# Kernel optimization log

Measured on AMD Instinct MI355X. Metric: run time of the kernel, lower is better.

The kernel has to match this reference:

```python
import jax, jax.numpy as jnp
import numpy as np

FR = 44100          # frame_rate
L = 882000          # sound length (20 s @ 44.1 kHz)
T = 2048            # number of onset time steps
H_GRU = 3
H_LSTM = 10


def setup_inputs() -> dict:
    key = jax.random.key(0)
    ks = jax.random.split(key, 20)

    def unif(k, shape, fan):
        b = 1.0 / np.sqrt(fan)
        return jax.random.uniform(k, shape, jnp.float32, -b, b)

    return {
        "sound": jax.random.normal(ks[0], (1, L), jnp.float32),
        "alpha": jnp.sort(jax.random.randint(ks[1], (1, T), 0, L), axis=1),
        # GRU (input_size=FR, hidden=3): gates ordered (r, z, n). W_hh is
        # multiplied by h0=0 (seq_len==1), so only its bias b_hh matters.
        "gru_w_ih": unif(ks[2], (3 * H_GRU, FR), H_GRU),
        "gru_b_ih": unif(ks[3], (3 * H_GRU,), H_GRU),
        "gru_b_hh": unif(ks[4], (3 * H_GRU,), H_GRU),
        "conv2_w": unif(ks[5], (32, 1, 3), 1 * 3),
        "conv2_b": unif(ks[6], (32,), 1 * 3),
        "conv3_w": unif(ks[7], (16, 32, 3), 32 * 3),
        "conv3_b": unif(ks[8], (16,), 32 * 3),
        "lin_w": unif(ks[9], (10, 17), 17),
        "lin_b": unif(ks[10], (10,), 17),
        # LSTMCell gates ordered (i, f, g, o)
        "lstm_w_ih": unif(ks[11], (4 * H_LSTM, 10), H_LSTM),
        "lstm_w_hh": unif(ks[12], (4 * H_LSTM, H_LSTM), H_LSTM),
        "lstm_b_ih": unif(ks[13], (4 * H_LSTM,), H_LSTM),
        "lstm_b_hh": unif(ks[14], (4 * H_LSTM,), H_LSTM),
        "lin1_w": unif(ks[15], (32, 10), 10),
        "lin1_b": unif(ks[16], (32,), 10),
        "lin2_w": unif(ks[17], (1, 32), 32),
        "lin2_b": unif(ks[18], (1,), 32),
    }


def _conv1d(x, w, b, pad):
    # x: (N, C_in, W), w: (C_out, C_in, K)
    y = jax.lax.conv_general_dilated(
        x, w, window_strides=(1,), padding=[(pad, pad)],
        dimension_numbers=("NCH", "OIH", "NCH"))
    return y + b[None, :, None]


def reference(sound, alpha, gru_w_ih, gru_b_ih, gru_b_hh,
              conv2_w, conv2_b, conv3_w, conv3_b, lin_w, lin_b,
              lstm_w_ih, lstm_w_hh, lstm_b_ih, lstm_b_hh,
              lin1_w, lin1_b, lin2_w, lin2_b):
    fr2 = FR // 2
    padded = jnp.pad(sound[0], (fr2, fr2))                       # (L + FR,)
    # Vectorized dynamic-window gather: one (T, FR) fragment matrix.
    idx = alpha[0][:, None] + jnp.arange(FR)[None, :]            # (T, FR)
    frags = jnp.abs(padded[idx])                                 # (T, FR)

    # GRU: batch=1 -> unbatched input of seq_len=1, h0=0 => single step.
    gi = frags @ gru_w_ih.T + gru_b_ih                           # (T, 9)
    r = jax.nn.sigmoid(gi[:, 0:3] + gru_b_hh[0:3])
    z = jax.nn.sigmoid(gi[:, 3:6] + gru_b_hh[3:6])
    n = jnp.tanh(gi[:, 6:9] + r * gru_b_hh[6:9])
    h = (1.0 - z) * n                                            # (T, 3)

    x = h[:, None, :]                                            # (T, 1, 3)
    x = jax.nn.relu(_conv1d(x, conv2_w, conv2_b, pad=1))         # (T, 32, 3)
    x = _conv1d(x, conv3_w, conv3_b, pad=0)                      # (T, 16, 1)
    feat = x[:, :, 0]                                            # (T, 16)

    a = alpha[0].astype(jnp.float32)
    intervals = jnp.concatenate([a[:1], a[1:] - a[:-1]])         # (T,)
    xin = jnp.concatenate([intervals[:, None], feat], axis=1)    # (T, 17)
    xin = xin @ lin_w.T + lin_b                                  # (T, 10)

    def step(carry, xt):
        hh, cc = carry
        g = xt @ lstm_w_ih.T + lstm_b_ih + hh @ lstm_w_hh.T + lstm_b_hh
        i, f, gg, o = jnp.split(g, 4)
        cc = jax.nn.sigmoid(f) * cc + jax.nn.sigmoid(i) * jnp.tanh(gg)
        hh = jax.nn.sigmoid(o) * jnp.tanh(cc)
        return (hh, cc), None

    init = (jnp.zeros(H_LSTM, jnp.float32), jnp.zeros(H_LSTM, jnp.float32))
    (hT, _), _ = jax.lax.scan(step, init, xin)                   # hT: (10,)

    y = jax.nn.relu(hT[None, :] @ lin1_w.T + lin1_b)             # (1, 32)
    return jax.nn.sigmoid(y @ lin2_w.T + lin2_b)                 # (1, 1)
```

## Files before the change

kernel.cpp:

```cpp
#include <hip/hip_runtime.h>

#define FRLEN 44100
#define FR2 22050
#define LSND 882000
#define PADLEN (LSND + FRLEN)
#define TSTEPS 2048
#define ROWS 8
#define NJ4 (FRLEN/4)
#define LOG2E 1.4426950408889634f

__device__ __forceinline__ float sigmoidf_(float x){ return 1.0f/(1.0f + __expf(-x)); }

__global__ void k_prep(const float* __restrict__ sound, float* __restrict__ padded){
  int stride = gridDim.x*blockDim.x;
  for (int i = blockIdx.x*blockDim.x + threadIdx.x; i < PADLEN; i += stride){
    int s = i - FR2;
    padded[i] = (s >= 0 && s < LSND) ? fabsf(sound[s]) : 0.0f;
  }
}

__global__ __launch_bounds__(512, 2) void k_gi(const float* __restrict__ padded,
                     const int* __restrict__ alpha,
                     const float* __restrict__ w,
                     float* __restrict__ gi_out){
  const int tid = threadIdx.x;
  const int row0 = blockIdx.x * ROWS;
  int base[ROWS];
#pragma unroll
  for (int r = 0; r < ROWS; ++r) base[r] = alpha[row0 + r];
  float acc[ROWS][9];
#pragma unroll
  for (int r = 0; r < ROWS; ++r)
#pragma unroll
    for (int k = 0; k < 9; ++k) acc[r][k] = 0.0f;

  for (int jj = tid; jj < NJ4; jj += 512){
    const int j = jj*4;
    float4 f[ROWS];
#pragma unroll
    for (int r = 0; r < ROWS; ++r)
      f[r] = *reinterpret_cast<const float4*>(padded + base[r] + j);
#pragma unroll
    for (int k = 0; k < 9; ++k){
      const float4 wv = *reinterpret_cast<const float4*>(w + k*FRLEN + j);
#pragma unroll
      for (int r = 0; r < ROWS; ++r){
        acc[r][k] = fmaf(f[r].x, wv.x, acc[r][k]);
        acc[r][k] = fmaf(f[r].y, wv.y, acc[r][k]);
        acc[r][k] = fmaf(f[r].z, wv.z, acc[r][k]);
        acc[r][k] = fmaf(f[r].w, wv.w, acc[r][k]);
      }
    }
  }
#pragma unroll
  for (int m = 32; m >= 1; m >>= 1){
#pragma unroll
    for (int r = 0; r < ROWS; ++r)
#pragma unroll
      for (int k = 0; k < 9; ++k)
        acc[r][k] += __shfl_xor(acc[r][k], m, 64);
  }
  __shared__ float red[8][ROWS*9];
  const int wv_ = tid >> 6, ln = tid & 63;
  if (ln == 0){
#pragma unroll
    for (int r = 0; r < ROWS; ++r)
#pragma unroll
      for (int k = 0; k < 9; ++k) red[wv_][r*9+k] = acc[r][k];
  }
  __syncthreads();
  if (tid < ROWS*9){
    float s = 0.0f;
#pragma unroll
    for (int q = 0; q < 8; ++q) s += red[q][tid];
    gi_out[row0*9 + tid] = s;
  }
}

__global__ void k_epi(const float* __restrict__ gi_in, const int* __restrict__ alpha,
    const float* __restrict__ gbih, const float* __restrict__ gbhh,
    const float* __restrict__ c2w, const float* __restrict__ c2b,
    const float* __restrict__ c3w, const float* __restrict__ c3b,
    const float* __restrict__ lw, const float* __restrict__ lb,
    const float* __restrict__ wih, const float* __restrict__ bih, const float* __restrict__ bhh,
    _Float16* __restrict__ pre){
  int t = blockIdx.x*blockDim.x + threadIdx.x;
  if (t >= TSTEPS) return;
  float gi[9];
#pragma unroll
  for (int k = 0; k < 9; ++k) gi[k] = gi_in[t*9+k] + gbih[k];
  float h[3];
#pragma unroll
  for (int q = 0; q < 3; ++q){
    float rr = sigmoidf_(gi[q]   + gbhh[q]);
    float zz = sigmoidf_(gi[3+q] + gbhh[3+q]);
    float nn = tanhf(gi[6+q] + rr*gbhh[6+q]);
    h[q] = (1.0f - zz)*nn;
  }
  float feat[16];
#pragma unroll
  for (int c = 0; c < 16; ++c) feat[c] = c3b[c];
  for (int ic = 0; ic < 32; ++ic){
    float w0 = c2w[ic*3+0], w1 = c2w[ic*3+1], w2 = c2w[ic*3+2], bb = c2b[ic];
    float x0 = fmaxf(bb + h[0]*w1 + h[1]*w2, 0.0f);
    float x1 = fmaxf(bb + h[0]*w0 + h[1]*w1 + h[2]*w2, 0.0f);
    float x2_ = fmaxf(bb + h[1]*w0 + h[2]*w1, 0.0f);
#pragma unroll
    for (int c = 0; c < 16; ++c){
      const float* wp = c3w + (c*32+ic)*3;
      feat[c] += x0*wp[0] + x1*wp[1] + x2_*wp[2];
    }
  }
  float interval = (float)(t == 0 ? alpha[0] : (alpha[t] - alpha[t-1]));
  float xin[10];
#pragma unroll
  for (int k = 0; k < 10; ++k){
    float s = lb[k] + interval*lw[k*17];
#pragma unroll
    for (int j = 0; j < 16; ++j) s = fmaf(feat[j], lw[k*17+1+j], s);
    xin[k] = s;
  }
#pragma unroll
  for (int k = 0; k < 40; ++k){
    float s = bih[k] + bhh[k];
#pragma unroll
    for (int i = 0; i < 10; ++i) s = fmaf(xin[i], wih[k*10+i], s);
    const float sc = (k >= 20 && k < 30) ? (-2.0f*LOG2E) : (-LOG2E);
    pre[t*40 + k] = (_Float16)(s * sc);
  }
}

#define LSTM_STEP(PREFETCH_STMT)                                              \
  {                                                                           \
    float g = (float)q0;                                                      \
    q0 = q1; q1 = q2; q2 = q3;                                                \
    PREFETCH_STMT;                                                            \
    float ga = g, gb = 0.0f;                                                  \
    _Pragma("unroll")                                                         \
    for (int i = 0; i < 5; ++i)  ga = fmaf(hs[i], w[i], ga);                  \
    _Pragma("unroll")                                                         \
    for (int i = 5; i < 10; ++i) gb = fmaf(hs[i], w[i], gb);                  \
    g = ga + gb;                                                              \
    float act = fmaf(__builtin_amdgcn_rcpf(1.0f + __builtin_amdgcn_exp2f(g)), s2, s3); \
    float g_sw = act;                                                         \
    asm("s_nop 1\n\tv_permlane32_swap_b32 %0, %1" : "+v"(act), "+v"(g_sw));   \
    float f_sw = act;                                                         \
    asm("v_permlane16_swap_b32 %0, %1" : "+v"(act), "+v"(f_sw));              \
    float o_sw = g_sw;                                                        \
    asm("v_permlane16_swap_b32 %0, %1" : "+v"(g_sw), "+v"(o_sw));             \
    float ig = act * g_sw;            \
    c = fmaf(f_sw, c, ig);                      \
    float th = fmaf(__builtin_amdgcn_rcpf(1.0f + __builtin_amdgcn_exp2f(c)), 2.0f, -1.0f); \
    float hn = o_sw * th;                                                     \
    _Pragma("unroll")                                                         \
    for (int i = 0; i < 10; ++i)                                              \
      hs[i] = __int_as_float(__builtin_amdgcn_readlane(__float_as_int(hn), i)); \
  }

__global__ __launch_bounds__(1024, 1) void k_lstm(const _Float16* __restrict__ pre,
                       const float* __restrict__ whh,
                       const float* __restrict__ l1w, const float* __restrict__ l1b,
                       const float* __restrict__ l2w, const float* __restrict__ l2b,
                       float* __restrict__ out){
  extern __shared__ _Float16 sp[];
  {
    uint4* dst = (uint4*)sp;
    const uint4* src = (const uint4*)pre;
    for (int i = threadIdx.x; i < (TSTEPS*40*2)/16; i += 1024) dst[i] = src[i];
  }
  __syncthreads();
  if (threadIdx.x >= 64) return;

  const int lane = threadIdx.x;
  const int gate = lane >> 4;
  const int unit_raw = lane & 15;
  const int unit = unit_raw < 10 ? unit_raw : 9;
  const int L40 = gate*10 + unit;
  const bool is_g = (gate == 2);
  const float kk  = -2.0f*LOG2E;
  const float wsc = is_g ? kk : (-LOG2E);
  const float s2  = is_g ? (2.0f*kk) : 1.0f;
  const float s3  = is_g ? (-kk)     : 0.0f;
  float w[10];
#pragma unroll
  for (int i = 0; i < 10; ++i) w[i] = whh[L40*10 + i] * wsc;

  float hs[10];
#pragma unroll
  for (int i = 0; i < 10; ++i) hs[i] = 0.0f;
  float c = 0.0f;

  _Float16 q0 = sp[0*40+L40], q1 = sp[1*40+L40], q2 = sp[2*40+L40], q3 = sp[3*40+L40];
#pragma unroll 4
  for (int t = 0; t < TSTEPS-4; ++t){
    LSTM_STEP(q3 = sp[(t+4)*40 + L40]);
  }
#pragma unroll
  for (int t = TSTEPS-4; t < TSTEPS; ++t){
    LSTM_STEP(;);
  }
  float z = 0.0f;
  if (lane < 32){
    float s = l1b[lane];
#pragma unroll
    for (int i = 0; i < 10; ++i) s = fmaf(hs[i], l1w[lane*10+i], s);
    z = fmaxf(s, 0.0f) * l2w[lane];
  }
#pragma unroll
  for (int m = 32; m >= 1; m >>= 1) z += __shfl_xor(z, m, 64);
  if (lane == 0) out[0] = sigmoidf_(z + l2b[0]);
}

extern "C" void kernel_launch(void* const* d_in, const int* in_sizes, int n_in,
                              void* d_out, int out_size, void* d_ws, size_t ws_size,
                              hipStream_t stream){
  const float* sound     = (const float*)d_in[0];
  const int*   alpha     = (const int*)  d_in[1];
  const float* gru_w_ih  = (const float*)d_in[2];
  const float* gru_b_ih  = (const float*)d_in[3];
  const float* gru_b_hh  = (const float*)d_in[4];
  const float* conv2_w   = (const float*)d_in[5];
  const float* conv2_b   = (const float*)d_in[6];
  const float* conv3_w   = (const float*)d_in[7];
  const float* conv3_b   = (const float*)d_in[8];
  const float* lin_w     = (const float*)d_in[9];
  const float* lin_b     = (const float*)d_in[10];
  const float* lstm_w_ih = (const float*)d_in[11];
  const float* lstm_w_hh = (const float*)d_in[12];
  const float* lstm_b_ih = (const float*)d_in[13];
  const float* lstm_b_hh = (const float*)d_in[14];
  const float* lin1_w    = (const float*)d_in[15];
  const float* lin1_b    = (const float*)d_in[16];
  const float* lin2_w    = (const float*)d_in[17];
  const float* lin2_b    = (const float*)d_in[18];

  float* padded = (float*)d_ws;
  float* gi     = padded + PADLEN;
  _Float16* pre = (_Float16*)(gi + TSTEPS*9);

  (void)hipFuncSetAttribute((const void*)k_lstm,
        hipFuncAttributeMaxDynamicSharedMemorySize, TSTEPS*40*2);

  hipLaunchKernelGGL(k_prep, dim3(2048), dim3(256), 0, stream, sound, padded);
  hipLaunchKernelGGL(k_gi, dim3(TSTEPS/ROWS), dim3(512), 0, stream, padded, alpha, gru_w_ih, gi);
  hipLaunchKernelGGL(k_epi, dim3(TSTEPS/256), dim3(256), 0, stream,
                     gi, alpha, gru_b_ih, gru_b_hh, conv2_w, conv2_b, conv3_w, conv3_b,
                     lin_w, lin_b, lstm_w_ih, lstm_b_ih, lstm_b_hh, pre);
  hipLaunchKernelGGL(k_lstm, dim3(1), dim3(1024), TSTEPS*40*2, stream,
                     pre, lstm_w_hh, lin1_w, lin1_b, lin2_w, lin2_b, (float*)d_out);
}
```

Measured before the change: 276.6 us.

## Convert GRU input projection to fp16 dot2 and fuse epilogue into gather kernel

Sound and GRU weights are pre-converted to packed fp16 pairs, with two copies of the sound (even- and odd-offset pairing) so that any alpha start offset can be read as aligned half2 pairs. The main gather-GEMV then uses fdot2 instructions, halving memory traffic and the FMA count. The GRU/conv/linear epilogue is fused into the same kernel, which removes one launch and the gi round trip. The LSTM asm has its s_nop padding tweaked. Using fp16 for the 44100-long dot products loses precision, and the per-row uint loads are scalar rather than vectorised.

```diff
diff --git a/kernel.cpp b/kernel.cpp
--- a/kernel.cpp
+++ b/kernel.cpp
@@ -6,127 +6,167 @@
 #define PADLEN (LSND + FRLEN)
 #define TSTEPS 2048
 #define ROWS 8
-#define NJ4 (FRLEN/4)
 #define LOG2E 1.4426950408889634f
 
+#define KPAD 44104
+#define WPROW (KPAD/2)
+#define NJP (WPROW/4)
+#define PAIRS 463056
+
+typedef _Float16 half2_ __attribute__((ext_vector_type(2)));
+
 __device__ __forceinline__ float sigmoidf_(float x){ return 1.0f/(1.0f + __expf(-x)); }
 
-__global__ void k_prep(const float* __restrict__ sound, float* __restrict__ padded){
-  int stride = gridDim.x*blockDim.x;
-  for (int i = blockIdx.x*blockDim.x + threadIdx.x; i < PADLEN; i += stride){
-    int s = i - FR2;
-    padded[i] = (s >= 0 && s < LSND) ? fabsf(sound[s]) : 0.0f;
-  }
-}
-
-__global__ __launch_bounds__(512, 2) void k_gi(const float* __restrict__ padded,
-                     const int* __restrict__ alpha,
-                     const float* __restrict__ w,
-                     float* __restrict__ gi_out){
-  const int tid = threadIdx.x;
-  const int row0 = blockIdx.x * ROWS;
-  int base[ROWS];
-#pragma unroll
-  for (int r = 0; r < ROWS; ++r) base[r] = alpha[row0 + r];
-  float acc[ROWS][9];
-#pragma unroll
-  for (int r = 0; r < ROWS; ++r)
-#pragma unroll
-    for (int k = 0; k < 9; ++k) acc[r][k] = 0.0f;
-
-  for (int jj = tid; jj < NJ4; jj += 512){
-    const int j = jj*4;
-    float4 f[ROWS];
-#pragma unroll
-    for (int r = 0; r < ROWS; ++r)
-      f[r] = *reinterpret_cast<const float4*>(padded + base[r] + j);
-#pragma unroll
-    for (int k = 0; k < 9; ++k){
-      const float4 wv = *reinterpret_cast<const float4*>(w + k*FRLEN + j);
-#pragma unroll
-      for (int r = 0; r < ROWS; ++r){
-        acc[r][k] = fmaf(f[r].x, wv.x, acc[r][k]);
-        acc[r][k] = fmaf(f[r].y, wv.y, acc[r][k]);
-        acc[r][k] = fmaf(f[r].z, wv.z, acc[r][k]);
-        acc[r][k] = fmaf(f[r].w, wv.w, acc[r][k]);
-      }
-    }
-  }
-#pragma unroll
-  for (int m = 32; m >= 1; m >>= 1){
-#pragma unroll
-    for (int r = 0; r < ROWS; ++r)
-#pragma unroll
-      for (int k = 0; k < 9; ++k)
-        acc[r][k] += __shfl_xor(acc[r][k], m, 64);
-  }
-  __shared__ float red[8][ROWS*9];
-  const int wv_ = tid >> 6, ln = tid & 63;
-  if (ln == 0){
-#pragma unroll
-    for (int r = 0; r < ROWS; ++r)
-#pragma unroll
-      for (int k = 0; k < 9; ++k) red[wv_][r*9+k] = acc[r][k];
-  }
-  __syncthreads();
-  if (tid < ROWS*9){
-    float s = 0.0f;
-#pragma unroll
-    for (int q = 0; q < 8; ++q) s += red[q][tid];
-    gi_out[row0*9 + tid] = s;
-  }
-}
-
-__global__ void k_epi(const float* __restrict__ gi_in, const int* __restrict__ alpha,
+__device__ __forceinline__ float dot2_(uint a, uint b, float c){
+#if __has_builtin(__builtin_amdgcn_fdot2)
+  return __builtin_amdgcn_fdot2(*(half2_*)&a, *(half2_*)&b, c, false);
+#else
+  half2_ ha = *(half2_*)&a, hb = *(half2_*)&b;
+  c = fmaf((float)ha.x, (float)hb.x, c);
+  return fmaf((float)ha.y, (float)hb.y, c);
+#endif
+}
+
+__global__ void k_prep16(const float* __restrict__ sound, const float* __restrict__ w,
+                         uint* __restrict__ pA, uint* __restrict__ pB,
+                         uint* __restrict__ wp){
+  const int stride = gridDim.x*blockDim.x;
+  for (int i = blockIdx.x*blockDim.x + threadIdx.x; i < PAIRS + 9*WPROW; i += stride){
+    if (i < PAIRS){
+      int e0 = 2*i - FR2;
+      float v0 = (e0 >= 0     && e0 < LSND)     ? fabsf(sound[e0])   : 0.0f;
+      float v1 = (e0+1 >= 0   && e0+1 < LSND)   ? fabsf(sound[e0+1]) : 0.0f;
+      float v2 = (e0+2 >= 0   && e0+2 < LSND)   ? fabsf(sound[e0+2]) : 0.0f;
+      half2_ a = { (_Float16)v0, (_Float16)v1 };
+      half2_ b = { (_Float16)v1, (_Float16)v2 };
+      pA[i] = *(uint*)&a;
+      pB[i] = *(uint*)&b;
+    } else {
+      int p = i - PAIRS;
+      int k = p / WPROW, pr = p % WPROW;
+      int j = 2*pr;
+      float v0 = (j   < FRLEN) ? w[k*FRLEN + j]   : 0.0f;
+      float v1 = (j+1 < FRLEN) ? w[k*FRLEN + j+1] : 0.0f;
+      half2_ a = { (_Float16)v0, (_Float16)v1 };
+      wp[i - PAIRS] = *(uint*)&a;
+    }
+  }
+}
+
+__global__ __launch_bounds__(512, 2) void k_front(const uint* __restrict__ pA,
+    const uint* __restrict__ pB, const uint* __restrict__ wp,
+    const int* __restrict__ alpha,
     const float* __restrict__ gbih, const float* __restrict__ gbhh,
     const float* __restrict__ c2w, const float* __restrict__ c2b,
     const float* __restrict__ c3w, const float* __restrict__ c3b,
     const float* __restrict__ lw, const float* __restrict__ lb,
     const float* __restrict__ wih, const float* __restrict__ bih, const float* __restrict__ bhh,
     _Float16* __restrict__ pre){
-  int t = blockIdx.x*blockDim.x + threadIdx.x;
-  if (t >= TSTEPS) return;
-  float gi[9];
-#pragma unroll
-  for (int k = 0; k < 9; ++k) gi[k] = gi_in[t*9+k] + gbih[k];
-  float h[3];
-#pragma unroll
-  for (int q = 0; q < 3; ++q){
-    float rr = sigmoidf_(gi[q]   + gbhh[q]);
-    float zz = sigmoidf_(gi[3+q] + gbhh[3+q]);
-    float nn = tanhf(gi[6+q] + rr*gbhh[6+q]);
-    h[q] = (1.0f - zz)*nn;
-  }
-  float feat[16];
-#pragma unroll
-  for (int c = 0; c < 16; ++c) feat[c] = c3b[c];
-  for (int ic = 0; ic < 32; ++ic){
-    float w0 = c2w[ic*3+0], w1 = c2w[ic*3+1], w2 = c2w[ic*3+2], bb = c2b[ic];
-    float x0 = fmaxf(bb + h[0]*w1 + h[1]*w2, 0.0f);
-    float x1 = fmaxf(bb + h[0]*w0 + h[1]*w1 + h[2]*w2, 0.0f);
-    float x2_ = fmaxf(bb + h[1]*w0 + h[2]*w1, 0.0f);
-#pragma unroll
-    for (int c = 0; c < 16; ++c){
-      const float* wp = c3w + (c*32+ic)*3;
-      feat[c] += x0*wp[0] + x1*wp[1] + x2_*wp[2];
-    }
-  }
-  float interval = (float)(t == 0 ? alpha[0] : (alpha[t] - alpha[t-1]));
-  float xin[10];
-#pragma unroll
-  for (int k = 0; k < 10; ++k){
-    float s = lb[k] + interval*lw[k*17];
-#pragma unroll
-    for (int j = 0; j < 16; ++j) s = fmaf(feat[j], lw[k*17+1+j], s);
-    xin[k] = s;
-  }
-#pragma unroll
-  for (int k = 0; k < 40; ++k){
-    float s = bih[k] + bhh[k];
-#pragma unroll
-    for (int i = 0; i < 10; ++i) s = fmaf(xin[i], wih[k*10+i], s);
-    const float sc = (k >= 20 && k < 30) ? (-2.0f*LOG2E) : (-LOG2E);
-    pre[t*40 + k] = (_Float16)(s * sc);
+  const int tid = threadIdx.x;
+  const int row0 = blockIdx.x * ROWS;
+  const uint* hp[ROWS];
+  int idx0[ROWS];
+#pragma unroll
+  for (int r = 0; r < ROWS; ++r){
+    int b = alpha[row0 + r];
+    hp[r] = (b & 1) ? pB : pA;
+    idx0[r] = b >> 1;
+  }
+  float acc[ROWS][9];
+#pragma unroll
+  for (int r = 0; r < ROWS; ++r)
+#pragma unroll
+    for (int k = 0; k < 9; ++k) acc[r][k] = 0.0f;
+
+  for (int jj = tid; jj < NJP; jj += 512){
+    const int jp = jj*4;
+    uint4 f[ROWS];
+#pragma unroll
+    for (int r = 0; r < ROWS; ++r){
+      const uint* p = hp[r] + idx0[r] + jp;
+      f[r].x = p[0]; f[r].y = p[1]; f[r].z = p[2]; f[r].w = p[3];
+    }
+#pragma unroll
+    for (int k = 0; k < 9; ++k){
+      const uint4 wq = *reinterpret_cast<const uint4*>(wp + k*WPROW + jp);
+#pragma unroll
+      for (int r = 0; r < ROWS; ++r){
+        acc[r][k] = dot2_(f[r].x, wq.x, acc[r][k]);
+        acc[r][k] = dot2_(f[r].y, wq.y, acc[r][k]);
+        acc[r][k] = dot2_(f[r].z, wq.z, acc[r][k]);
+        acc[r][k] = dot2_(f[r].w, wq.w, acc[r][k]);
+      }
+    }
+  }
+#pragma unroll
+  for (int m = 32; m >= 1; m >>= 1){
+#pragma unroll
+    for (int r = 0; r < ROWS; ++r)
+#pragma unroll
+      for (int k = 0; k < 9; ++k)
+        acc[r][k] += __shfl_xor(acc[r][k], m, 64);
+  }
+  __shared__ float red[8][ROWS*9];
+  __shared__ float sgi[ROWS*9];
+  const int wv_ = tid >> 6, ln = tid & 63;
+  if (ln == 0){
+#pragma unroll
+    for (int r = 0; r < ROWS; ++r)
+#pragma unroll
+      for (int k = 0; k < 9; ++k) red[wv_][r*9+k] = acc[r][k];
+  }
+  __syncthreads();
+  if (tid < ROWS*9){
+    float s = 0.0f;
+#pragma unroll
+    for (int q = 0; q < 8; ++q) s += red[q][tid];
+    sgi[tid] = s;
+  }
+  __syncthreads();
+  if (tid < ROWS){
+    const int t = row0 + tid;
+    float gi[9];
+#pragma unroll
+    for (int k = 0; k < 9; ++k) gi[k] = sgi[tid*9+k] + gbih[k];
+    float h[3];
+#pragma unroll
+    for (int q = 0; q < 3; ++q){
+      float rr = sigmoidf_(gi[q]   + gbhh[q]);
+      float zz = sigmoidf_(gi[3+q] + gbhh[3+q]);
+      float nn = tanhf(gi[6+q] + rr*gbhh[6+q]);
+      h[q] = (1.0f - zz)*nn;
+    }
+    float feat[16];
+#pragma unroll
+    for (int c = 0; c < 16; ++c) feat[c] = c3b[c];
+    for (int ic = 0; ic < 32; ++ic){
+      float w0 = c2w[ic*3+0], w1 = c2w[ic*3+1], w2 = c2w[ic*3+2], bb = c2b[ic];
+      float x0 = fmaxf(bb + h[0]*w1 + h[1]*w2, 0.0f);
+      float x1 = fmaxf(bb + h[0]*w0 + h[1]*w1 + h[2]*w2, 0.0f);
+      float x2_ = fmaxf(bb + h[1]*w0 + h[2]*w1, 0.0f);
+#pragma unroll
+      for (int c = 0; c < 16; ++c){
+        const float* wpp = c3w + (c*32+ic)*3;
+        feat[c] += x0*wpp[0] + x1*wpp[1] + x2_*wpp[2];
+      }
+    }
+    float interval = (float)(t == 0 ? alpha[0] : (alpha[t] - alpha[t-1]));
+    float xin[10];
+#pragma unroll
+    for (int k = 0; k < 10; ++k){
+      float s = lb[k] + interval*lw[k*17];
+#pragma unroll
+      for (int j = 0; j < 16; ++j) s = fmaf(feat[j], lw[k*17+1+j], s);
+      xin[k] = s;
+    }
+#pragma unroll
+    for (int k = 0; k < 40; ++k){
+      float s = bih[k] + bhh[k];
+#pragma unroll
+      for (int i = 0; i < 10; ++i) s = fmaf(xin[i], wih[k*10+i], s);
+      const float sc = (k >= 20 && k < 30) ? (-2.0f*LOG2E) : (-LOG2E);
+      pre[t*40 + k] = (_Float16)(s * sc);
+    }
   }
 }
 
@@ -143,13 +183,13 @@
     g = ga + gb;                                                              \
     float act = fmaf(__builtin_amdgcn_rcpf(1.0f + __builtin_amdgcn_exp2f(g)), s2, s3); \
     float g_sw = act;                                                         \
-    asm("s_nop 1\n\tv_permlane32_swap_b32 %0, %1" : "+v"(act), "+v"(g_sw));   \
+    asm("s_nop 0\n\tv_permlane32_swap_b32 %0, %1" : "+v"(act), "+v"(g_sw));   \
     float f_sw = act;                                                         \
     asm("v_permlane16_swap_b32 %0, %1" : "+v"(act), "+v"(f_sw));              \
     float o_sw = g_sw;                                                        \
-    asm("v_permlane16_swap_b32 %0, %1" : "+v"(g_sw), "+v"(o_sw));             \
-    float ig = act * g_sw;            \
-    c = fmaf(f_sw, c, ig);                      \
+    asm("s_nop 0\n\tv_permlane16_swap_b32 %0, %1" : "+v"(g_sw), "+v"(o_sw));  \
+    float ig = act * g_sw;                                                    \
+    c = fmaf(f_sw, c, ig);                                                    \
     float th = fmaf(__builtin_amdgcn_rcpf(1.0f + __builtin_amdgcn_exp2f(c)), 2.0f, -1.0f); \
     float hn = o_sw * th;                                                     \
     _Pragma("unroll")                                                         \
@@ -234,17 +274,20 @@
   const float* lin2_w    = (const float*)d_in[17];
   const float* lin2_b    = (const float*)d_in[18];
 
-  float* padded = (float*)d_ws;
-  float* gi     = padded + PADLEN;
-  _Float16* pre = (_Float16*)(gi + TSTEPS*9);
+  char* ws = (char*)d_ws;
+  uint* pA      = (uint*)ws;
+  uint* pB      = pA + PAIRS;
+  uint* wpairs  = pB + PAIRS;
+  _Float16* pre = (_Float16*)(wpairs + 9*WPROW);
 
   (void)hipFuncSetAttribute((const void*)k_lstm,
         hipFuncAttributeMaxDynamicSharedMemorySize, TSTEPS*40*2);
 
-  hipLaunchKernelGGL(k_prep, dim3(2048), dim3(256), 0, stream, sound, padded);
-  hipLaunchKernelGGL(k_gi, dim3(TSTEPS/ROWS), dim3(512), 0, stream, padded, alpha, gru_w_ih, gi);
-  hipLaunchKernelGGL(k_epi, dim3(TSTEPS/256), dim3(256), 0, stream,
-                     gi, alpha, gru_b_ih, gru_b_hh, conv2_w, conv2_b, conv3_w, conv3_b,
+  hipLaunchKernelGGL(k_prep16, dim3(1536), dim3(256), 0, stream,
+                     sound, gru_w_ih, pA, pB, wpairs);
+  hipLaunchKernelGGL(k_front, dim3(TSTEPS/ROWS), dim3(512), 0, stream,
+                     pA, pB, wpairs, alpha,
+                     gru_b_ih, gru_b_hh, conv2_w, conv2_b, conv3_w, conv3_b,
                      lin_w, lin_b, lstm_w_ih, lstm_b_ih, lstm_b_hh, pre);
   hipLaunchKernelGGL(k_lstm, dim3(1), dim3(1024), TSTEPS*40*2, stream,
                      pre, lstm_w_hh, lin1_w, lin1_b, lin2_w, lin2_b, (float*)d_out);
```

Result: faster. 260.8 us (-5.7%).
